# Performance work log

Measured on AMD Instinct MI355X. Metric: run time of the kernel, lower is better.

## Reference

```python
import jax, jax.numpy as jnp
import numpy as np

S, B, D = 2048, 1, 4096
H, HKV, DH = 32, 8, 128
THETA = 10000.0


def _rope_tables(seq_len, dim, theta):
    inv_freq = 1.0 / (theta ** (jnp.arange(0, dim, 2, dtype=jnp.float32) / dim))
    freqs = jnp.arange(seq_len, dtype=jnp.float32)[:, None] * inv_freq[None, :]  # [S, DH/2]
    return jnp.cos(freqs), jnp.sin(freqs)


def _apply_rope(x, cos, sin):
    # x: [B, H, S, DH]; non-interleaved (flash_attn interleaved=False) rotation
    half = x.shape[-1] // 2
    x1, x2 = x[..., :half], x[..., half:]
    c = cos[None, None, :, :]
    s = sin[None, None, :, :]
    return jnp.concatenate([x1 * c - x2 * s, x2 * c + x1 * s], axis=-1)


def setup_inputs() -> dict:
    key = jax.random.key(0)
    k1, k2, k3 = jax.random.split(key, 3)
    hidden_states = jax.random.normal(k1, (S, B, D), dtype=jnp.float32)
    W_qkv = jax.random.normal(k2, (D, (H + 2 * HKV) * DH), dtype=jnp.float32) * 0.02
    W_o = jax.random.normal(k3, (H * DH, D), dtype=jnp.float32) * 0.02
    sequence_mask = jnp.ones((B, S), dtype=jnp.int32)
    return {"hidden_states": hidden_states, "sequence_mask": sequence_mask,
            "W_qkv": W_qkv, "W_o": W_o}


def reference(hidden_states, sequence_mask, W_qkv, W_o):
    s, b, _ = hidden_states.shape
    qkv = hidden_states @ W_qkv  # [S, B, (H+2*HKV)*DH]
    q, k, v = jnp.split(qkv, [H * DH, H * DH + HKV * DH], axis=-1)
    q = q.reshape(s, b, H, DH).transpose(1, 2, 0, 3)    # [B, H, S, DH]
    k = k.reshape(s, b, HKV, DH).transpose(1, 2, 0, 3)  # [B, HKV, S, DH]
    v = v.reshape(s, b, HKV, DH).transpose(1, 2, 0, 3)

    cos, sin = _rope_tables(s, DH, THETA)
    q = _apply_rope(q, cos, sin)
    k = _apply_rope(k, cos, sin)

    # GQA: repeat kv heads
    rep = H // HKV
    k = jnp.repeat(k, rep, axis=1)  # [B, H, S, DH]
    v = jnp.repeat(v, rep, axis=1)

    scale = 1.0 / jnp.sqrt(jnp.asarray(DH, dtype=q.dtype))
    scores = jnp.einsum('bhqd,bhkd->bhqk', q, k) * scale
    causal = jnp.tril(jnp.ones((s, s), dtype=bool))
    scores = jnp.where(causal[None, None, :, :], scores, jnp.finfo(scores.dtype).min)
    attn = jax.nn.softmax(scores, axis=-1)
    ctx = jnp.einsum('bhqk,bhkd->bhqd', attn, v)  # [B, H, S, DH]
    ctx = ctx.transpose(2, 0, 1, 3).reshape(s, b, H * DH)  # [S, B, H*DH]
    out = ctx @ W_o  # [S, B, D]
    return out
```

## Files before the change

kernel.cpp:

```cpp
#include <hip/hip_runtime.h>

typedef unsigned short u16;
typedef __bf16 bf16x8 __attribute__((ext_vector_type(8)));
typedef float f32x4 __attribute__((ext_vector_type(4)));
typedef u16 u16x4 __attribute__((ext_vector_type(4)));

constexpr int SEQ = 2048;
constexpr int NQKV = 6144;

__device__ __forceinline__ float bf2f(u16 x) {
    unsigned int u = ((unsigned int)x) << 16;
    return __builtin_bit_cast(float, u);
}
__device__ __forceinline__ u16 f2bf(float f) {
    unsigned int u = __builtin_bit_cast(unsigned int, f);
    u += 0x7FFF + ((u >> 16) & 1);
    return (u16)(u >> 16);
}

__device__ __forceinline__ void gload16(const void* g, void* l) {
    void* gg = const_cast<void*>(g);
    __builtin_amdgcn_global_load_lds(
        (__attribute__((address_space(1))) void*)gg,
        (__attribute__((address_space(3))) void*)l, 16, 0, 0);
}

__device__ __forceinline__ void gatebar(int G) {
    if (G == 4) asm volatile("s_waitcnt vmcnt(4)" ::: "memory");
    else if (G == 3) asm volatile("s_waitcnt vmcnt(3)" ::: "memory");
    else if (G == 2) asm volatile("s_waitcnt vmcnt(2)" ::: "memory");
    else asm volatile("s_waitcnt vmcnt(0)" ::: "memory");
    __builtin_amdgcn_sched_barrier(0);
    __builtin_amdgcn_s_barrier();
    __builtin_amdgcn_sched_barrier(0);
}

__global__ void rope_table_k(float* __restrict__ tab) {
    int idx = blockIdx.x * 256 + threadIdx.x;
    if (idx >= SEQ * 64) return;
    int s = idx >> 6;
    int i = idx & 63;
    float invf = expf(-(float)i * (float)(1.0 / 64.0) * logf(10000.0f));
    float ang = (float)s * invf;
    float sv, cv;
    sincosf(ang, &sv, &cv);
    tab[idx * 2] = cv;
    tab[idx * 2 + 1] = sv;
}

__global__ __launch_bounds__(256) void cast_k(const float* __restrict__ src,
                                              u16* __restrict__ dst, int n4) {
    int i = blockIdx.x * 256 + threadIdx.x;
    if (i >= n4) return;
    f32x4 v = *(const f32x4*)&src[(size_t)i * 4];
    u16x4 o;
#pragma unroll
    for (int j = 0; j < 4; ++j) o[j] = f2bf(v[j]);
    *(u16x4*)&dst[(size_t)i * 4] = o;
}

__global__ __launch_bounds__(256) void transpose_cast_k(const float* __restrict__ src,
                                                        u16* __restrict__ dst, int R, int C) {
    __shared__ u16 tile[64][65];
    int t = threadIdx.x;
    int bx = blockIdx.x, by = blockIdx.y;
    int r0 = by * 64, c0 = bx * 64;
#pragma unroll
    for (int it = 0; it < 4; ++it) {
        int row = it * 16 + (t >> 4);
        int col = (t & 15) * 4;
        f32x4 v = *(const f32x4*)&src[(size_t)(r0 + row) * C + c0 + col];
        tile[row][col] = f2bf(v[0]); tile[row][col + 1] = f2bf(v[1]);
        tile[row][col + 2] = f2bf(v[2]); tile[row][col + 3] = f2bf(v[3]);
    }
    __syncthreads();
#pragma unroll
    for (int it = 0; it < 4; ++it) {
        int orow = it * 16 + (t >> 4);
        int ocol = (t & 15) * 4;
        u16x4 v;
        v[0] = tile[ocol][orow]; v[1] = tile[ocol + 1][orow];
        v[2] = tile[ocol + 2][orow]; v[3] = tile[ocol + 3][orow];
        *(u16x4*)&dst[(size_t)(c0 + orow) * R + r0 + ocol] = v;
    }
}

__global__ __launch_bounds__(512, 2) void gemm1_big_k(const u16* __restrict__ A,
                                                      const u16* __restrict__ BT,
                                                      u16* __restrict__ C) {
    constexpr int K = 4096, N = 6144;
    constexpr int SBUF = 57344;
    __shared__ alignas(16) char lds[2 * SBUF];

    int t = threadIdx.x;
    int lane = t & 63, w = t >> 6;
    int wr = w >> 2, wc = w & 3;
    int l15 = lane & 15, l4 = lane >> 4;

    int wg = blockIdx.x;
    int xcd = wg & 7, j = wg >> 3;
    int bm = ((xcd >> 2) << 2) + (j >> 3);
    int bn = ((xcd & 3) << 3) + (j & 7);

    const u16* Ab = A + (size_t)bm * 256 * K;
    const u16* Bb = BT + (size_t)bn * 192 * K;

    const u16* ga[4]; int da[4];
#pragma unroll
    for (int i = 0; i < 4; ++i) {
        int c = t + i * 512;
        int row = c >> 3;
        int ch = (c & 7) ^ (row & 7);
        ga[i] = Ab + (size_t)row * K + ch * 8;
        da[i] = c * 16;
    }
    const u16* gb[3]; int db[3];
#pragma unroll
    for (int i = 0; i < 3; ++i) {
        int c = t + i * 512;
        int row = c >> 3;
        int ch = (c & 7) ^ (row & 7);
        gb[i] = Bb + (size_t)row * K + ch * 8;
        db[i] = 32768 + c * 16;
    }

    auto stage = [&](int kt) {
        char* L = lds + (kt & 1) * SBUF;
        int ko = kt * 64;
#pragma unroll
        for (int i = 0; i < 4; ++i) gload16(ga[i] + ko, L + da[i]);
#pragma unroll
        for (int i = 0; i < 3; ++i) gload16(gb[i] + ko, L + db[i]);
    };

    f32x4 acc[8][3];
#pragma unroll
    for (int i = 0; i < 8; ++i)
#pragma unroll
        for (int j2 = 0; j2 < 3; ++j2) acc[i][j2] = f32x4{0.f, 0.f, 0.f, 0.f};

    int arow[8];
#pragma unroll
    for (int fm = 0; fm < 8; ++fm) arow[fm] = wr * 128 + fm * 16 + l15;
    int brow[3];
#pragma unroll
    for (int fn = 0; fn < 3; ++fn) brow[fn] = wc * 48 + fn * 16 + l15;

    stage(0);
    gatebar(0);

    for (int kt = 0; kt < 64; ++kt) {
        const u16* L = (const u16*)(lds + (kt & 1) * SBUF);
        if (kt + 1 < 64) stage(kt + 1);
        bf16x8 bf[3][2];
#pragma unroll
        for (int fn = 0; fn < 3; ++fn)
#pragma unroll
            for (int kk = 0; kk < 2; ++kk) {
                int ch = (kk * 4 + l4) ^ (brow[fn] & 7);
                bf[fn][kk] = *(const bf16x8*)&L[16384 + brow[fn] * 64 + ch * 8];
            }
#pragma unroll
        for (int p = 0; p < 4; ++p) {
            bf16x8 af[2][2];
#pragma unroll
            for (int f2 = 0; f2 < 2; ++f2)
#pragma unroll
                for (int kk = 0; kk < 2; ++kk) {
                    int r = arow[p * 2 + f2];
                    int ch = (kk * 4 + l4) ^ (r & 7);
                    af[f2][kk] = *(const bf16x8*)&L[r * 64 + ch * 8];
                }
            __builtin_amdgcn_s_setprio(1);
#pragma unroll
            for (int f2 = 0; f2 < 2; ++f2)
#pragma unroll
                for (int kk = 0; kk < 2; ++kk)
#pragma unroll
                    for (int fn = 0; fn < 3; ++fn)
                        acc[p * 2 + f2][fn] = __builtin_amdgcn_mfma_f32_16x16x32_bf16(
                            af[f2][kk], bf[fn][kk], acc[p * 2 + f2][fn], 0, 0, 0);
            __builtin_amdgcn_s_setprio(0);
        }
        gatebar(0);
    }

#pragma unroll
    for (int fm = 0; fm < 8; ++fm)
#pragma unroll
        for (int fn = 0; fn < 3; ++fn)
#pragma unroll
            for (int i = 0; i < 4; ++i) {
                int row = bm * 256 + wr * 128 + fm * 16 + l4 * 4 + i;
                int col = bn * 192 + wc * 48 + fn * 16 + l15;
                C[(size_t)row * N + col] = f2bf(acc[fm][fn][i]);
            }
}

__global__ __launch_bounds__(512, 2) void gemm2_big_k(const u16* __restrict__ A,
                                                      const u16* __restrict__ BT,
                                                      float* __restrict__ C) {
    constexpr int K = 4096, N = 4096;
    constexpr int SBUF = 49152;
    __shared__ alignas(16) char lds[2 * SBUF];

    int t = threadIdx.x;
    int lane = t & 63, w = t >> 6;
    int wr = w >> 2, wc = w & 3;
    int l15 = lane & 15, l4 = lane >> 4;

    int wg = blockIdx.x;
    int xcd = wg & 7, j = wg >> 3;
    int bm = ((xcd >> 2) << 2) + (j >> 3);
    int bn = ((xcd & 3) << 3) + (j & 7);

    const u16* Ab = A + (size_t)bm * 256 * K;
    const u16* Bb = BT + (size_t)bn * 128 * K;

    const u16* ga[4]; int da[4];
#pragma unroll
    for (int i = 0; i < 4; ++i) {
        int c = t + i * 512;
        int row = c >> 3;
        int ch = (c & 7) ^ (row & 7);
        ga[i] = Ab + (size_t)row * K + ch * 8;
        da[i] = c * 16;
    }
    const u16* gb[2]; int db[2];
#pragma unroll
    for (int i = 0; i < 2; ++i) {
        int c = t + i * 512;
        int row = c >> 3;
        int ch = (c & 7) ^ (row & 7);
        gb[i] = Bb + (size_t)row * K + ch * 8;
        db[i] = 32768 + c * 16;
    }

    auto stage = [&](int kt) {
        char* L = lds + (kt & 1) * SBUF;
        int ko = kt * 64;
#pragma unroll
        for (int i = 0; i < 4; ++i) gload16(ga[i] + ko, L + da[i]);
#pragma unroll
        for (int i = 0; i < 2; ++i) gload16(gb[i] + ko, L + db[i]);
    };

    f32x4 acc[8][2];
#pragma unroll
    for (int i = 0; i < 8; ++i)
#pragma unroll
        for (int j2 = 0; j2 < 2; ++j2) acc[i][j2] = f32x4{0.f, 0.f, 0.f, 0.f};

    int arow[8];
#pragma unroll
    for (int fm = 0; fm < 8; ++fm) arow[fm] = wr * 128 + fm * 16 + l15;
    int brow[2];
#pragma unroll
    for (int fn = 0; fn < 2; ++fn) brow[fn] = wc * 32 + fn * 16 + l15;

    stage(0);
    gatebar(0);

    for (int kt = 0; kt < 64; ++kt) {
        const u16* L = (const u16*)(lds + (kt & 1) * SBUF);
        if (kt + 1 < 64) stage(kt + 1);
        bf16x8 bf[2][2];
#pragma unroll
        for (int fn = 0; fn < 2; ++fn)
#pragma unroll
            for (int kk = 0; kk < 2; ++kk) {
                int ch = (kk * 4 + l4) ^ (brow[fn] & 7);
                bf[fn][kk] = *(const bf16x8*)&L[16384 + brow[fn] * 64 + ch * 8];
            }
#pragma unroll
        for (int p = 0; p < 4; ++p) {
            bf16x8 af[2][2];
#pragma unroll
            for (int f2 = 0; f2 < 2; ++f2)
#pragma unroll
                for (int kk = 0; kk < 2; ++kk) {
                    int r = arow[p * 2 + f2];
                    int ch = (kk * 4 + l4) ^ (r & 7);
                    af[f2][kk] = *(const bf16x8*)&L[r * 64 + ch * 8];
                }
            __builtin_amdgcn_s_setprio(1);
#pragma unroll
            for (int f2 = 0; f2 < 2; ++f2)
#pragma unroll
                for (int kk = 0; kk < 2; ++kk)
#pragma unroll
                    for (int fn = 0; fn < 2; ++fn)
                        acc[p * 2 + f2][fn] = __builtin_amdgcn_mfma_f32_16x16x32_bf16(
                            af[f2][kk], bf[fn][kk], acc[p * 2 + f2][fn], 0, 0, 0);
            __builtin_amdgcn_s_setprio(0);
        }
        gatebar(0);
    }

#pragma unroll
    for (int fm = 0; fm < 8; ++fm)
#pragma unroll
        for (int fn = 0; fn < 2; ++fn)
#pragma unroll
            for (int i = 0; i < 4; ++i) {
                int row = bm * 256 + wr * 128 + fm * 16 + l4 * 4 + i;
                int col = bn * 128 + wc * 32 + fn * 16 + l15;
                C[(size_t)row * N + col] = acc[fm][fn][i];
            }
}

__global__ __launch_bounds__(256) void repack_rope_k(const u16* __restrict__ QKV,
                                                     const float* __restrict__ tab,
                                                     u16* __restrict__ Qo, u16* __restrict__ Ko,
                                                     u16* __restrict__ Vo) {
    int idx = blockIdx.x * 256 + threadIdx.x;
    int i4 = (idx & 15) * 4;
    int su = idx >> 4;
    int u = su % 48;
    int s = su / 48;
    if (u < 40) {
        const float* tp = tab + (s * 64 + i4) * 2;
        f32x4 t0 = *(const f32x4*)tp;
        f32x4 t1 = *(const f32x4*)(tp + 4);
        float cv[4] = {t0[0], t0[2], t1[0], t1[2]};
        float sv[4] = {t0[1], t0[3], t1[1], t1[3]};
        const u16* base;
        u16* ob;
        if (u < 32) {
            base = QKV + (size_t)s * NQKV + u * 128;
            ob = Qo + ((size_t)u * SEQ + s) * 128;
        } else {
            base = QKV + (size_t)s * NQKV + 4096 + (u - 32) * 128;
            ob = Ko + ((size_t)(u - 32) * SEQ + s) * 128;
        }
        u16x4 x1 = *(const u16x4*)(base + i4);
        u16x4 x2 = *(const u16x4*)(base + 64 + i4);
        u16x4 o1, o2;
#pragma unroll
        for (int j = 0; j < 4; ++j) {
            float a = bf2f(x1[j]), b = bf2f(x2[j]);
            o1[j] = f2bf(a * cv[j] - b * sv[j]);
            o2[j] = f2bf(b * cv[j] + a * sv[j]);
        }
        *(u16x4*)(ob + i4) = o1;
        *(u16x4*)(ob + 64 + i4) = o2;
    } else {
        int hv = u - 40;
        const u16* base = QKV + (size_t)s * NQKV + 5120 + hv * 128;
        u16* ob = Vo + ((size_t)hv * SEQ + s) * 128;
        *(u16x4*)(ob + i4) = *(const u16x4*)(base + i4);
        *(u16x4*)(ob + 64 + i4) = *(const u16x4*)(base + 64 + i4);
    }
}

__global__ __launch_bounds__(512) void attn_k(const u16* __restrict__ Qg,
                                              const u16* __restrict__ Kg,
                                              const u16* __restrict__ Vg,
                                              u16* __restrict__ ctx) {
    constexpr float SCL2 = 0.08838834764831845f * 1.44269504088896340736f;
    constexpr float THR = 11.5f;
    __shared__ alignas(16) u16 Klds[2][64 * 128];
    __shared__ alignas(16) u16 VT[2][128 * 72];
    __shared__ alignas(16) u16 Plds[8 * 16 * 72];

    int t = threadIdx.x;
    int lane = t & 63, w = t >> 6;
    int l15 = lane & 15, l4 = lane >> 4;
    int bx = blockIdx.x;
    int h = blockIdx.y, hkv = h >> 2;
    const u16* Kh = Kg + (size_t)hkv * SEQ * 128;
    const u16* Vh = Vg + (size_t)hkv * SEQ * 128;
    u16* Pw = &Plds[w * 1152];

    int kr[2], kchs[2];
#pragma unroll
    for (int i2 = 0; i2 < 2; ++i2) {
        int c = t + i2 * 512;
        kr[i2] = c >> 4;
        kchs[i2] = (c & 15) ^ (kr[i2] & 7);
    }
    int vr = lane, vcb = (t >> 6) * 16;

    int q0 = bx * 128;
    int ntA = 2 * bx + 2;

    bf16x8 qf[4], vreg[2];
    f32x4 o[8];
    float m_i[4], l_i[4];

    auto kvbase = [&](int tt) { return (tt < ntA ? tt : tt - ntA) << 6; };
    auto load_q = [&]() {
        const u16* Qh = Qg + ((size_t)h * SEQ + q0 + w * 16 + l15) * 128;
#pragma unroll
        for (int ks = 0; ks < 4; ++ks) qf[ks] = *(const bf16x8*)(Qh + ks * 32 + l4 * 8);
    };
    auto reset_acc = [&]() {
#pragma unroll
        for (int nf = 0; nf < 8; ++nf) o[nf] = f32x4{0.f, 0.f, 0.f, 0.f};
#pragma unroll
        for (int i = 0; i < 4; ++i) { m_i[i] = -3.0e38f; l_i[i] = 0.f; }
    };
    auto write_ctx = [&]() {
        float inv[4];
#pragma unroll
        for (int i = 0; i < 4; ++i) {
            float rs = l_i[i];
            rs += __shfl_xor(rs, 1);
            rs += __shfl_xor(rs, 2);
            rs += __shfl_xor(rs, 4);
            rs += __shfl_xor(rs, 8);
            inv[i] = 1.0f / rs;
        }
#pragma unroll
        for (int nf = 0; nf < 8; ++nf)
#pragma unroll
            for (int i = 0; i < 4; ++i) {
                int qrow = q0 + w * 16 + l4 * 4 + i;
                ctx[(size_t)qrow * 4096 + h * 128 + nf * 16 + l15] = f2bf(o[nf][i] * inv[i]);
            }
    };
    auto loadV = [&](int tt) {
        const u16* Vt = Vh + (size_t)kvbase(tt) * 128;
#pragma unroll
        for (int seg = 0; seg < 2; ++seg)
            vreg[seg] = *(const bf16x8*)(Vt + (size_t)vr * 128 + vcb + seg * 8);
    };
    auto stageK = [&](int tt) {
        const u16* Kt = Kh + (size_t)kvbase(tt) * 128;
        char* kb = (char*)Klds[tt & 1];
#pragma unroll
        for (int i2 = 0; i2 < 2; ++i2)
            gload16(Kt + kr[i2] * 128 + kchs[i2] * 8, kb + (size_t)(t + i2 * 512) * 16);
    };
    auto writeV = [&](int tt) {
        u16* vb = VT[tt & 1];
#pragma unroll
        for (int seg = 0; seg < 2; ++seg) {
            int c0 = vcb + seg * 8;
            u16* vv = (u16*)&vreg[seg];
#pragma unroll
            for (int j = 0; j < 8; ++j) vb[(c0 + j) * 72 + vr] = vv[j];
        }
    };

    load_q();
    reset_acc();
    loadV(0);
    stageK(0);
    asm volatile("s_waitcnt vmcnt(0)" ::: "memory");
    __builtin_amdgcn_sched_barrier(0);
    writeV(0);

    for (int tt = 0; tt < 34; ++tt) {
        asm volatile("s_waitcnt lgkmcnt(0)" ::: "memory");
        __builtin_amdgcn_sched_barrier(0);
        __builtin_amdgcn_s_barrier();
        __builtin_amdgcn_sched_barrier(0);
        bool nxt = (tt + 1 < 34);
        if (nxt) {
            loadV(tt + 1);
            stageK(tt + 1);
        }
        gatebar(nxt ? 4 : 0);
        if (tt == ntA) {
            write_ctx();
            q0 = (15 - bx) * 128;
            load_q();
            reset_acc();
        }

        int b = tt & 1;
        int kv0 = kvbase(tt);
        const u16* KL = Klds[b];

        f32x4 sa[4];
#pragma unroll
        for (int cg = 0; cg < 4; ++cg) {
            sa[cg] = f32x4{0.f, 0.f, 0.f, 0.f};
            int row = cg * 16 + l15;
#pragma unroll
            for (int ks = 0; ks < 4; ++ks) {
                int chs = (ks * 4 + l4) ^ (row & 7);
                bf16x8 kf = *(const bf16x8*)&KL[row * 128 + chs * 8];
                sa[cg] = __builtin_amdgcn_mfma_f32_16x16x32_bf16(qf[ks], kf, sa[cg], 0, 0, 0);
            }
        }
#pragma unroll
        for (int cg = 0; cg < 4; ++cg)
#pragma unroll
            for (int i = 0; i < 4; ++i) sa[cg][i] *= SCL2;
        if (kv0 + 63 > q0 + w * 16) {
#pragma unroll
            for (int cg = 0; cg < 4; ++cg) {
                int col = kv0 + cg * 16 + l15;
#pragma unroll
                for (int i = 0; i < 4; ++i) {
                    int qrow = q0 + w * 16 + l4 * 4 + i;
                    if (col > qrow) sa[cg][i] = -3.0e38f;
                }
            }
        }
        float lmx[4];
#pragma unroll
        for (int i = 0; i < 4; ++i)
            lmx[i] = fmaxf(fmaxf(sa[0][i], sa[1][i]), fmaxf(sa[2][i], sa[3][i]));
        bool defer = __all((lmx[0] <= m_i[0] + THR) & (lmx[1] <= m_i[1] + THR) &
                           (lmx[2] <= m_i[2] + THR) & (lmx[3] <= m_i[3] + THR));
        if (!defer) {
            float corr[4];
#pragma unroll
            for (int i = 0; i < 4; ++i) {
                float m0 = lmx[i];
                m0 = fmaxf(m0, __shfl_xor(m0, 1));
                m0 = fmaxf(m0, __shfl_xor(m0, 2));
                m0 = fmaxf(m0, __shfl_xor(m0, 4));
                m0 = fmaxf(m0, __shfl_xor(m0, 8));
                float mnew = fmaxf(m_i[i], m0);
                corr[i] = __builtin_amdgcn_exp2f(m_i[i] - mnew);
                m_i[i] = mnew;
                l_i[i] *= corr[i];
            }
#pragma unroll
            for (int nf = 0; nf < 8; ++nf) {
                o[nf][0] *= corr[0]; o[nf][1] *= corr[1];
                o[nf][2] *= corr[2]; o[nf][3] *= corr[3];
            }
        }
        if (nxt) writeV(tt + 1);
#pragma unroll
        for (int i = 0; i < 4; ++i) {
            int prow = l4 * 4 + i;
            int sw = (prow >> 1) & 3;
            float rs = 0.f;
#pragma unroll
            for (int cg = 0; cg < 4; ++cg) {
                float p = __builtin_amdgcn_exp2f(sa[cg][i] - m_i[i]);
                rs += p;
                int ch = cg * 2 + (l15 >> 3);
                Pw[prow * 72 + ((ch ^ sw) << 3) + (l15 & 7)] = f2bf(p);
            }
            l_i[i] += rs;
        }
        asm volatile("s_waitcnt lgkmcnt(0)" ::: "memory");
        __builtin_amdgcn_sched_barrier(0);
#pragma unroll
        for (int kst = 0; kst < 2; ++kst) {
            int pchs = (kst * 4 + l4) ^ ((l15 >> 1) & 3);
            bf16x8 pf = *(const bf16x8*)&Pw[l15 * 72 + pchs * 8];
#pragma unroll
            for (int nf = 0; nf < 8; ++nf) {
                bf16x8 vf = *(const bf16x8*)&VT[b][(nf * 16 + l15) * 72 + kst * 32 + l4 * 8];
                o[nf] = __builtin_amdgcn_mfma_f32_16x16x32_bf16(pf, vf, o[nf], 0, 0, 0);
            }
        }
    }
    write_ctx();
}

extern "C" void kernel_launch(void* const* d_in, const int* in_sizes, int n_in,
                              void* d_out, int out_size, void* d_ws, size_t ws_size,
                              hipStream_t stream) {
    const float* hidden = (const float*)d_in[0];
    const float* Wqkv = (const float*)d_in[2];
    const float* Wo = (const float*)d_in[3];
    float* out = (float*)d_out;
    char* ws = (char*)d_ws;

    u16* WqkvT   = (u16*)(ws + 0);
    u16* Qb      = (u16*)(ws + 0);
    u16* Kb      = (u16*)(ws + 16777216);
    u16* Vb      = (u16*)(ws + 20971520);
    u16* WoT     = (u16*)(ws + 25165824);
    u16* QKV     = (u16*)(ws + 50331648);
    u16* ctx     = (u16*)(ws + 58720256);
    float* tab   = (float*)(ws + 75497472);
    u16* hiddenB = (u16*)(ws + 76546048);

    rope_table_k<<<512, 256, 0, stream>>>(tab);
    cast_k<<<8192, 256, 0, stream>>>(hidden, hiddenB, 2048 * 4096 / 4);
    transpose_cast_k<<<dim3(96, 64), 256, 0, stream>>>(Wqkv, WqkvT, 4096, 6144);
    gemm1_big_k<<<256, 512, 0, stream>>>(hiddenB, WqkvT, QKV);
    repack_rope_k<<<6144, 256, 0, stream>>>(QKV, tab, Qb, Kb, Vb);
    transpose_cast_k<<<dim3(64, 64), 256, 0, stream>>>(Wo, WoT, 4096, 4096);
    attn_k<<<dim3(8, 32), 512, 0, stream>>>(Qb, Kb, Vb, ctx);
    gemm2_big_k<<<256, 512, 0, stream>>>(ctx, WoT, out);
}
```

Before: 325.7 us.

## Pre-transpose V globally and stage it into LDS with async direct loads

Adds a separate kernel that writes V in a transposed [head, dim, seq] layout, and drops V from the repack kernel. The attention kernel now loads V tiles with global_load_lds into an XOR-swizzled LDS buffer, in the same way as K. This replaces the per-tile register load and scattered transposing LDS writes, and removes one waitcnt/barrier pair per iteration. In exchange it adds an extra kernel launch and one more pass over V in global memory.

```diff
diff --git a/kernel.cpp b/kernel.cpp
--- a/kernel.cpp
+++ b/kernel.cpp
@@ -85,6 +85,35 @@
     }
 }
 
+__global__ __launch_bounds__(256) void transpose_vt_k(const u16* __restrict__ QKV,
+                                                      u16* __restrict__ VTg) {
+    __shared__ u16 tile[64][65];
+    int t = threadIdx.x;
+    int s0 = blockIdx.x * 64;
+    int hv = blockIdx.y >> 1;
+    int d0 = (blockIdx.y & 1) * 64;
+    const u16* src = QKV + (size_t)s0 * NQKV + 5120 + hv * 128 + d0;
+#pragma unroll
+    for (int it = 0; it < 4; ++it) {
+        int row = it * 16 + (t >> 4);
+        int col = (t & 15) * 4;
+        u16x4 v = *(const u16x4*)&src[(size_t)row * NQKV + col];
+        tile[row][col] = v[0]; tile[row][col + 1] = v[1];
+        tile[row][col + 2] = v[2]; tile[row][col + 3] = v[3];
+    }
+    __syncthreads();
+    u16* dst = VTg + (size_t)hv * 128 * SEQ + (size_t)d0 * SEQ + s0;
+#pragma unroll
+    for (int it = 0; it < 4; ++it) {
+        int orow = it * 16 + (t >> 4);
+        int ocol = (t & 15) * 4;
+        u16x4 v;
+        v[0] = tile[ocol][orow]; v[1] = tile[ocol + 1][orow];
+        v[2] = tile[ocol + 2][orow]; v[3] = tile[ocol + 3][orow];
+        *(u16x4*)&dst[(size_t)orow * SEQ + ocol] = v;
+    }
+}
+
 __global__ __launch_bounds__(512, 2) void gemm1_big_k(const u16* __restrict__ A,
                                                       const u16* __restrict__ BT,
                                                       u16* __restrict__ C) {
@@ -311,56 +340,47 @@
 
 __global__ __launch_bounds__(256) void repack_rope_k(const u16* __restrict__ QKV,
                                                      const float* __restrict__ tab,
-                                                     u16* __restrict__ Qo, u16* __restrict__ Ko,
-                                                     u16* __restrict__ Vo) {
+                                                     u16* __restrict__ Qo, u16* __restrict__ Ko) {
     int idx = blockIdx.x * 256 + threadIdx.x;
     int i4 = (idx & 15) * 4;
     int su = idx >> 4;
-    int u = su % 48;
-    int s = su / 48;
-    if (u < 40) {
-        const float* tp = tab + (s * 64 + i4) * 2;
-        f32x4 t0 = *(const f32x4*)tp;
-        f32x4 t1 = *(const f32x4*)(tp + 4);
-        float cv[4] = {t0[0], t0[2], t1[0], t1[2]};
-        float sv[4] = {t0[1], t0[3], t1[1], t1[3]};
-        const u16* base;
-        u16* ob;
-        if (u < 32) {
-            base = QKV + (size_t)s * NQKV + u * 128;
-            ob = Qo + ((size_t)u * SEQ + s) * 128;
-        } else {
-            base = QKV + (size_t)s * NQKV + 4096 + (u - 32) * 128;
-            ob = Ko + ((size_t)(u - 32) * SEQ + s) * 128;
-        }
-        u16x4 x1 = *(const u16x4*)(base + i4);
-        u16x4 x2 = *(const u16x4*)(base + 64 + i4);
-        u16x4 o1, o2;
-#pragma unroll
-        for (int j = 0; j < 4; ++j) {
-            float a = bf2f(x1[j]), b = bf2f(x2[j]);
-            o1[j] = f2bf(a * cv[j] - b * sv[j]);
-            o2[j] = f2bf(b * cv[j] + a * sv[j]);
-        }
-        *(u16x4*)(ob + i4) = o1;
-        *(u16x4*)(ob + 64 + i4) = o2;
+    int u = su % 40;
+    int s = su / 40;
+    const float* tp = tab + (s * 64 + i4) * 2;
+    f32x4 t0 = *(const f32x4*)tp;
+    f32x4 t1 = *(const f32x4*)(tp + 4);
+    float cv[4] = {t0[0], t0[2], t1[0], t1[2]};
+    float sv[4] = {t0[1], t0[3], t1[1], t1[3]};
+    const u16* base;
+    u16* ob;
+    if (u < 32) {
+        base = QKV + (size_t)s * NQKV + u * 128;
+        ob = Qo + ((size_t)u * SEQ + s) * 128;
     } else {
-        int hv = u - 40;
-        const u16* base = QKV + (size_t)s * NQKV + 5120 + hv * 128;
-        u16* ob = Vo + ((size_t)hv * SEQ + s) * 128;
-        *(u16x4*)(ob + i4) = *(const u16x4*)(base + i4);
-        *(u16x4*)(ob + 64 + i4) = *(const u16x4*)(base + 64 + i4);
-    }
+        base = QKV + (size_t)s * NQKV + 4096 + (u - 32) * 128;
+        ob = Ko + ((size_t)(u - 32) * SEQ + s) * 128;
+    }
+    u16x4 x1 = *(const u16x4*)(base + i4);
+    u16x4 x2 = *(const u16x4*)(base + 64 + i4);
+    u16x4 o1, o2;
+#pragma unroll
+    for (int j = 0; j < 4; ++j) {
+        float a = bf2f(x1[j]), b = bf2f(x2[j]);
+        o1[j] = f2bf(a * cv[j] - b * sv[j]);
+        o2[j] = f2bf(b * cv[j] + a * sv[j]);
+    }
+    *(u16x4*)(ob + i4) = o1;
+    *(u16x4*)(ob + 64 + i4) = o2;
 }
 
 __global__ __launch_bounds__(512) void attn_k(const u16* __restrict__ Qg,
                                               const u16* __restrict__ Kg,
-                                              const u16* __restrict__ Vg,
+                                              const u16* __restrict__ VTg,
                                               u16* __restrict__ ctx) {
     constexpr float SCL2 = 0.08838834764831845f * 1.44269504088896340736f;
     constexpr float THR = 11.5f;
     __shared__ alignas(16) u16 Klds[2][64 * 128];
-    __shared__ alignas(16) u16 VT[2][128 * 72];
+    __shared__ alignas(16) u16 VTl[2][128 * 64];
     __shared__ alignas(16) u16 Plds[8 * 16 * 72];
 
     int t = threadIdx.x;
@@ -369,7 +389,7 @@
     int bx = blockIdx.x;
     int h = blockIdx.y, hkv = h >> 2;
     const u16* Kh = Kg + (size_t)hkv * SEQ * 128;
-    const u16* Vh = Vg + (size_t)hkv * SEQ * 128;
+    const u16* Vh = VTg + (size_t)hkv * 128 * SEQ;
     u16* Pw = &Plds[w * 1152];
 
     int kr[2], kchs[2];
@@ -379,12 +399,18 @@
         kr[i2] = c >> 4;
         kchs[i2] = (c & 15) ^ (kr[i2] & 7);
     }
-    int vr = lane, vcb = (t >> 6) * 16;
+    int vd[2], vchs[2];
+#pragma unroll
+    for (int i2 = 0; i2 < 2; ++i2) {
+        int c = t + i2 * 512;
+        vd[i2] = c >> 3;
+        vchs[i2] = (c & 7) ^ (vd[i2] & 7);
+    }
 
     int q0 = bx * 128;
     int ntA = 2 * bx + 2;
 
-    bf16x8 qf[4], vreg[2];
+    bf16x8 qf[4];
     f32x4 o[8];
     float m_i[4], l_i[4];
 
@@ -419,48 +445,29 @@
                 ctx[(size_t)qrow * 4096 + h * 128 + nf * 16 + l15] = f2bf(o[nf][i] * inv[i]);
             }
     };
-    auto loadV = [&](int tt) {
-        const u16* Vt = Vh + (size_t)kvbase(tt) * 128;
-#pragma unroll
-        for (int seg = 0; seg < 2; ++seg)
-            vreg[seg] = *(const bf16x8*)(Vt + (size_t)vr * 128 + vcb + seg * 8);
-    };
-    auto stageK = [&](int tt) {
-        const u16* Kt = Kh + (size_t)kvbase(tt) * 128;
+    auto stage = [&](int tt) {
+        int kv0 = kvbase(tt);
+        const u16* Kt = Kh + (size_t)kv0 * 128;
         char* kb = (char*)Klds[tt & 1];
+        char* vb = (char*)VTl[tt & 1];
 #pragma unroll
         for (int i2 = 0; i2 < 2; ++i2)
             gload16(Kt + kr[i2] * 128 + kchs[i2] * 8, kb + (size_t)(t + i2 * 512) * 16);
-    };
-    auto writeV = [&](int tt) {
-        u16* vb = VT[tt & 1];
-#pragma unroll
-        for (int seg = 0; seg < 2; ++seg) {
-            int c0 = vcb + seg * 8;
-            u16* vv = (u16*)&vreg[seg];
-#pragma unroll
-            for (int j = 0; j < 8; ++j) vb[(c0 + j) * 72 + vr] = vv[j];
-        }
+#pragma unroll
+        for (int i2 = 0; i2 < 2; ++i2)
+            gload16(Vh + (size_t)vd[i2] * SEQ + kv0 + vchs[i2] * 8,
+                    vb + (size_t)(t + i2 * 512) * 16);
     };
 
     load_q();
     reset_acc();
-    loadV(0);
-    stageK(0);
-    asm volatile("s_waitcnt vmcnt(0)" ::: "memory");
-    __builtin_amdgcn_sched_barrier(0);
-    writeV(0);
+    stage(0);
 
     for (int tt = 0; tt < 34; ++tt) {
-        asm volatile("s_waitcnt lgkmcnt(0)" ::: "memory");
-        __builtin_amdgcn_sched_barrier(0);
         __builtin_amdgcn_s_barrier();
         __builtin_amdgcn_sched_barrier(0);
         bool nxt = (tt + 1 < 34);
-        if (nxt) {
-            loadV(tt + 1);
-            stageK(tt + 1);
-        }
+        if (nxt) stage(tt + 1);
         gatebar(nxt ? 4 : 0);
         if (tt == ntA) {
             write_ctx();
@@ -472,6 +479,7 @@
         int b = tt & 1;
         int kv0 = kvbase(tt);
         const u16* KL = Klds[b];
+        const u16* VL = VTl[b];
 
         f32x4 sa[4];
 #pragma unroll
@@ -526,7 +534,6 @@
                 o[nf][2] *= corr[2]; o[nf][3] *= corr[3];
             }
         }
-        if (nxt) writeV(tt + 1);
 #pragma unroll
         for (int i = 0; i < 4; ++i) {
             int prow = l4 * 4 + i;
@@ -549,7 +556,9 @@
             bf16x8 pf = *(const bf16x8*)&Pw[l15 * 72 + pchs * 8];
 #pragma unroll
             for (int nf = 0; nf < 8; ++nf) {
-                bf16x8 vf = *(const bf16x8*)&VT[b][(nf * 16 + l15) * 72 + kst * 32 + l4 * 8];
+                int d = nf * 16 + l15;
+                int vch = (kst * 4 + l4) ^ (d & 7);
+                bf16x8 vf = *(const bf16x8*)&VL[d * 64 + vch * 8];
                 o[nf] = __builtin_amdgcn_mfma_f32_16x16x32_bf16(pf, vf, o[nf], 0, 0, 0);
             }
         }
@@ -569,7 +578,7 @@
     u16* WqkvT   = (u16*)(ws + 0);
     u16* Qb      = (u16*)(ws + 0);
     u16* Kb      = (u16*)(ws + 16777216);
-    u16* Vb      = (u16*)(ws + 20971520);
+    u16* VTg     = (u16*)(ws + 20971520);
     u16* WoT     = (u16*)(ws + 25165824);
     u16* QKV     = (u16*)(ws + 50331648);
     u16* ctx     = (u16*)(ws + 58720256);
@@ -580,8 +589,9 @@
     cast_k<<<8192, 256, 0, stream>>>(hidden, hiddenB, 2048 * 4096 / 4);
     transpose_cast_k<<<dim3(96, 64), 256, 0, stream>>>(Wqkv, WqkvT, 4096, 6144);
     gemm1_big_k<<<256, 512, 0, stream>>>(hiddenB, WqkvT, QKV);
-    repack_rope_k<<<6144, 256, 0, stream>>>(QKV, tab, Qb, Kb, Vb);
+    repack_rope_k<<<5120, 256, 0, stream>>>(QKV, tab, Qb, Kb);
+    transpose_vt_k<<<dim3(32, 16), 256, 0, stream>>>(QKV, VTg);
     transpose_cast_k<<<dim3(64, 64), 256, 0, stream>>>(Wo, WoT, 4096, 4096);
-    attn_k<<<dim3(8, 32), 512, 0, stream>>>(Qb, Kb, Vb, ctx);
+    attn_k<<<dim3(8, 32), 512, 0, stream>>>(Qb, Kb, VTg, ctx);
     gemm2_big_k<<<256, 512, 0, stream>>>(ctx, WoT, out);
 }
```

New measurement: 311.4 us. 1.05x faster.
